# Performance work log

Measured on AMD Instinct MI355X. Metric: run time of the kernel, lower is better.

## Reference

```python
import jax, jax.numpy as jnp
import numpy as np

B, S, E = 2, 2048, 1024
H = 16
D = E // H          # head_dim = 64
W = 32              # sliding window / block size


def setup_inputs() -> dict:
    key = jax.random.key(0)
    k1, k2, k3 = jax.random.split(key, 3)
    x = jax.random.normal(k1, (B, S, E), dtype=jnp.float32)
    # xavier-uniform-like scale for the projections
    lim_qkv = float(np.sqrt(6.0 / (E + 3 * E)))
    lim_o = float(np.sqrt(6.0 / (E + E)))
    Wqkv = jax.random.uniform(k2, (3 * E, E), minval=-lim_qkv, maxval=lim_qkv, dtype=jnp.float32)
    bqkv = jnp.zeros((3 * E,), dtype=jnp.float32)
    Wo = jax.random.uniform(k3, (E, E), minval=-lim_o, maxval=lim_o, dtype=jnp.float32)
    bo = jnp.zeros((E,), dtype=jnp.float32)
    return {"x": x, "Wqkv": Wqkv, "bqkv": bqkv, "Wo": Wo, "bo": bo}


def _roll_blocks(kb, w):
    # kb: (BH, nb, w, d). Replicates roll(): w circularly-shifted copies along the
    # block axis, original inserted at index (w-1)//2, concatenated within-block.
    shifts = list(range(1, w))
    shifts.insert((w - 1) // 2, 0)
    return jnp.concatenate([jnp.roll(kb, s, axis=1) for s in shifts], axis=2)  # (BH, nb, w*w, d)


def reference(x, Wqkv, bqkv, Wo, bo):
    b, s, e = x.shape
    qkv = x @ Wqkv.T + bqkv                              # (B,S,3E)
    qkv = qkv.reshape(b, s, H, 3 * D).transpose(0, 2, 1, 3)  # (B,H,S,3D)
    q, k, v = jnp.split(qkv, 3, axis=-1)                 # each (B,H,S,D)

    nb = s // W
    qb = q.reshape(b * H, nb, W, D)
    kb = k.reshape(b * H, nb, W, D)
    kblk = _roll_blocks(kb, W)                           # (BH, nb, W*W, D)
    qk = jnp.einsum('bcxd,bcyd->bcxy', qb, kblk)         # (BH, nb, W, W*W)
    attn = qk.reshape(b, H, s, W * W) / jnp.sqrt(jnp.float32(D))
    attn = jax.nn.softmax(attn, axis=-1)
    # Faithful to torch.einsum('ijkl,ijkm->ijkm', attn, v): sum attn over its
    # last axis (==1 after softmax) and broadcast-multiply v.
    vals = attn.sum(axis=-1, keepdims=True) * v          # (B,H,S,D)

    vals = vals.transpose(0, 2, 1, 3).reshape(b, s, e)   # (B,S,E)
    return vals @ Wo.T + bo
```

## Files before the change

kernel.cpp:

```cpp
#include <hip/hip_runtime.h>
#include <hip/hip_bf16.h>
#include <type_traits>

#define MROWS 4096
#define EDIM  1024

typedef __attribute__((ext_vector_type(8))) __bf16 bf16x8;
typedef __attribute__((ext_vector_type(4))) float f32x4;
typedef __attribute__((ext_vector_type(8))) unsigned short ushort8;

__device__ __forceinline__ unsigned short f2bf(float f) {
    unsigned u = __builtin_bit_cast(unsigned, f);
    u += 0x7FFFu + ((u >> 16) & 1u);
    return (unsigned short)(u >> 16);
}

__device__ __forceinline__ void async_load16(const void* g, void* l) {
    __builtin_amdgcn_global_load_lds(
        (const __attribute__((address_space(1))) void*)g,
        (__attribute__((address_space(3))) void*)l, 16, 0, 0);
}

__device__ __forceinline__ void cast8(const float* __restrict__ in,
                                      unsigned short* __restrict__ out, int i) {
    const float4* p = (const float4*)in + (size_t)i * 2;
    float4 a = p[0], b = p[1];
    ushort8 r;
    r[0] = f2bf(a.x); r[1] = f2bf(a.y); r[2] = f2bf(a.z); r[3] = f2bf(a.w);
    r[4] = f2bf(b.x); r[5] = f2bf(b.y); r[6] = f2bf(b.z); r[7] = f2bf(b.w);
    *((ushort8*)out + i) = r;
}

template<bool BIAS, typename OUT_T, int MD, int ND, int KD,
         int BM, int BN, int BK, int NWM, int NWN>
__device__ __forceinline__ void gemm_bt_body(
    const unsigned short* __restrict__ A, const unsigned short* __restrict__ B,
    OUT_T* __restrict__ C, const float* __restrict__ bias, int id,
    unsigned short* sm)
{
    constexpr int THREADS = NWM * NWN * 64;
    constexpr int NBM = MD / BM, NBN = ND / BN, NWG = NBM * NBN;
    constexpr int CPX = NWG / 8;
    constexpr int WTM = BM / NWM, WTN = BN / NWN;
    constexpr int AM = WTM / 16, AN = WTN / 16;
    constexpr int CHUNKS = BK / 8;
    constexpr int RPP = THREADS / CHUNKS;
    constexpr int TILE = (BM + BN) * BK;

    const int t = threadIdx.x;
    const int swz = (id & 7) * CPX + (id >> 3);
    const int bm = swz % NBM, bn = swz / NBM;

    const int lane = t & 63, wave = t >> 6;
    const int wr = wave / NWN, wc = wave % NWN;

    const int rsub = t / CHUNKS;
    const int kb   = (t % CHUNKS) * 8;

    const unsigned short* Ag = A + (size_t)(bm * BM + rsub) * KD + kb;
    const unsigned short* Bg = B + (size_t)(bn * BN + rsub) * KD + kb;

    f32x4 acc[AM][AN] = {};

    auto stage = [&](int buf, int k0) {
        unsigned short* As = sm + buf * TILE;
        unsigned short* Bs = As + BM * BK;
        #pragma unroll
        for (int p = 0; p < BM / RPP; ++p)
            async_load16(Ag + (size_t)(p * RPP) * KD + k0, &As[(rsub + p * RPP) * BK + kb]);
        #pragma unroll
        for (int p = 0; p < BN / RPP; ++p)
            async_load16(Bg + (size_t)(p * RPP) * KD + k0, &Bs[(rsub + p * RPP) * BK + kb]);
    };

    auto compute = [&](int buf) {
        const unsigned short* As = sm + buf * TILE;
        const unsigned short* Bs = As + BM * BK;
        #pragma unroll
        for (int ks = 0; ks < BK / 32; ++ks) {
            bf16x8 a[AM], b[AN];
            #pragma unroll
            for (int mi = 0; mi < AM; ++mi)
                a[mi] = *(const bf16x8*)&As[(wr * WTM + mi * 16 + (lane & 15)) * BK + ks * 32 + (lane >> 4) * 8];
            #pragma unroll
            for (int ni = 0; ni < AN; ++ni)
                b[ni] = *(const bf16x8*)&Bs[(wc * WTN + ni * 16 + (lane & 15)) * BK + ks * 32 + (lane >> 4) * 8];
            #pragma unroll
            for (int mi = 0; mi < AM; ++mi)
                #pragma unroll
                for (int ni = 0; ni < AN; ++ni)
                    acc[mi][ni] = __builtin_amdgcn_mfma_f32_16x16x32_bf16(
                        a[mi], b[ni], acc[mi][ni], 0, 0, 0);
        }
    };

    stage(0, 0);
    __syncthreads();
    int cur = 0;
    for (int k0 = BK; k0 < KD; k0 += BK) {
        stage(cur ^ 1, k0);
        compute(cur);
        __syncthreads();
        cur ^= 1;
    }
    compute(cur);

    const int crow0 = bm * BM + wr * WTM + (lane >> 4) * 4;
    const int ccol0 = bn * BN + wc * WTN + (lane & 15);
    #pragma unroll
    for (int mi = 0; mi < AM; ++mi) {
        #pragma unroll
        for (int ni = 0; ni < AN; ++ni) {
            const int col = ccol0 + ni * 16;
            float bv = 0.f;
            if constexpr (BIAS) bv = bias[col];
            #pragma unroll
            for (int i = 0; i < 4; ++i) {
                const int row = crow0 + mi * 16 + i;
                float val = acc[mi][ni][i] + bv;
                if constexpr (std::is_same<OUT_T, float>::value)
                    C[(size_t)row * ND + col] = val;
                else
                    C[(size_t)row * ND + col] = f2bf(val);
            }
        }
    }
}

__global__ __launch_bounds__(256) void prep_w(
    const float* __restrict__ Wqkv, const float* __restrict__ bqkv,
    const float* __restrict__ Wo, const float* __restrict__ bo,
    unsigned short* __restrict__ WvT, unsigned short* __restrict__ wo_bf,
    float* __restrict__ c)
{
    const int blk = blockIdx.x;
    const int t = threadIdx.x;
    if (blk < 256) {
        __shared__ unsigned short tile[64][65];
        const int eBase = (blk & 15) * 64, kBase = (blk >> 4) * 64;
        const int tx = t & 63, ty = t >> 6;
        #pragma unroll
        for (int r = ty; r < 64; r += 4) {
            int k = kBase + r;
            int j = ((k >> 6) * 192) + 128 + (k & 63);
            tile[r][tx] = f2bf(Wqkv[(size_t)j * EDIM + eBase + tx]);
        }
        __syncthreads();
        #pragma unroll
        for (int r = ty; r < 64; r += 4)
            WvT[(size_t)(eBase + r) * EDIM + kBase + tx] = tile[tx][r];
    } else if (blk < 768) {
        cast8(Wo, wo_bf, (blk - 256) * 256 + t);
    } else {
        const int b = blk - 768;
        const int wave = t >> 6, lane = t & 63;
        for (int r = 0; r < 16; ++r) {
            int row = b * 64 + wave * 16 + r;
            float s = 0.f;
            #pragma unroll
            for (int kk = 0; kk < 16; ++kk) {
                int k = kk * 64 + lane;
                int j = kk * 192 + 128 + lane;
                s += Wo[(size_t)row * EDIM + k] * bqkv[j];
            }
            #pragma unroll
            for (int off = 32; off > 0; off >>= 1) s += __shfl_down(s, off);
            if (lane == 0) c[row] = s + bo[row];
        }
    }
}

__global__ __launch_bounds__(256, 2) void gemm1_castx(
    const unsigned short* __restrict__ wo_bf, const unsigned short* __restrict__ wvt,
    unsigned short* __restrict__ m_bf,
    const float* __restrict__ x, unsigned short* __restrict__ x_bf)
{
    __shared__ unsigned short smem[2 * (64 + 64) * 64];
    const int blk = blockIdx.x;
    if (blk < 256) {
        gemm_bt_body<false, unsigned short, EDIM, EDIM, EDIM, 64, 64, 64, 2, 2>(
            wo_bf, wvt, m_bf, nullptr, blk, smem);
    } else {
        cast8(x, x_bf, (blk - 256) * 256 + threadIdx.x);
    }
}

__global__ __launch_bounds__(256, 2) void gemm2(
    const unsigned short* __restrict__ x_bf, const unsigned short* __restrict__ m_bf,
    float* __restrict__ out, const float* __restrict__ cvec)
{
    __shared__ unsigned short smem[2 * (128 + 64) * 64];
    gemm_bt_body<true, float, MROWS, EDIM, EDIM, 128, 64, 64, 2, 2>(
        x_bf, m_bf, out, cvec, blockIdx.x, smem);
}

extern "C" void kernel_launch(void* const* d_in, const int* in_sizes, int n_in,
                              void* d_out, int out_size, void* d_ws, size_t ws_size,
                              hipStream_t stream) {
    const float* x    = (const float*)d_in[0];
    const float* Wqkv = (const float*)d_in[1];
    const float* bqkv = (const float*)d_in[2];
    const float* Wo   = (const float*)d_in[3];
    const float* bo   = (const float*)d_in[4];
    float* out = (float*)d_out;

    char* ws = (char*)d_ws;
    unsigned short* x_bf  = (unsigned short*)(ws);
    unsigned short* wvt   = (unsigned short*)(ws + 8u  * 1024 * 1024);
    unsigned short* wo_bf = (unsigned short*)(ws + 10u * 1024 * 1024);
    unsigned short* m_bf  = (unsigned short*)(ws + 12u * 1024 * 1024);
    float*          cvec  = (float*)(ws + 14u * 1024 * 1024);

    prep_w<<<784, 256, 0, stream>>>(Wqkv, bqkv, Wo, bo, wvt, wo_bf, cvec);
    gemm1_castx<<<2304, 256, 0, stream>>>(wo_bf, wvt, m_bf, x, x_bf);
    gemm2<<<512, 256, 0, stream>>>(x_bf, m_bf, out, cvec);
}
```

Before: 47.47 us.

## Triple-buffer GEMM LDS pipeline with explicit vmcnt waits

Replaces the double-buffered global-to-LDS load loop with a three-stage ring that issues loads two tiles ahead. It waits with explicit s_waitcnt vmcnt counts instead of __syncthreads, so later tiles stay in flight while the current one is computed. This is meant to hide global load latency behind MFMA work. In exchange LDS use per block grows by half, which may lower occupancy, and correctness depends on the hand-computed vmcnt literals matching the number of issued loads.

```diff
diff --git a/kernel.cpp b/kernel.cpp
--- a/kernel.cpp
+++ b/kernel.cpp
@@ -19,6 +19,15 @@
     __builtin_amdgcn_global_load_lds(
         (const __attribute__((address_space(1))) void*)g,
         (__attribute__((address_space(3))) void*)l, 16, 0, 0);
+}
+
+template<int N> __device__ __forceinline__ void wait_vmcnt() {
+    if constexpr (N == 0)       asm volatile("s_waitcnt vmcnt(0)" ::: "memory");
+    else if constexpr (N == 4)  asm volatile("s_waitcnt vmcnt(4)" ::: "memory");
+    else if constexpr (N == 6)  asm volatile("s_waitcnt vmcnt(6)" ::: "memory");
+    else if constexpr (N == 8)  asm volatile("s_waitcnt vmcnt(8)" ::: "memory");
+    else if constexpr (N == 12) asm volatile("s_waitcnt vmcnt(12)" ::: "memory");
+    else static_assert(N < 0, "unsupported vmcnt literal");
 }
 
 __device__ __forceinline__ void cast8(const float* __restrict__ in,
@@ -46,6 +55,8 @@
     constexpr int CHUNKS = BK / 8;
     constexpr int RPP = THREADS / CHUNKS;
     constexpr int TILE = (BM + BN) * BK;
+    constexpr int L = BM / RPP + BN / RPP;
+    constexpr int NIT = KD / BK;
 
     const int t = threadIdx.x;
     const int swz = (id & 7) * CPX + (id >> 3);
@@ -95,15 +106,21 @@
     };
 
     stage(0, 0);
-    __syncthreads();
-    int cur = 0;
-    for (int k0 = BK; k0 < KD; k0 += BK) {
-        stage(cur ^ 1, k0);
-        compute(cur);
-        __syncthreads();
-        cur ^= 1;
-    }
-    compute(cur);
+    stage(1, BK);
+
+    for (int it = 0; it < NIT; ++it) {
+        __builtin_amdgcn_s_barrier();
+        if (it + 2 < NIT) {
+            stage((it + 2) % 3, (it + 2) * BK);
+            wait_vmcnt<2 * L>();
+        } else if (it + 1 < NIT) {
+            wait_vmcnt<L>();
+        } else {
+            wait_vmcnt<0>();
+        }
+        __builtin_amdgcn_s_barrier();
+        compute(it % 3);
+    }
 
     const int crow0 = bm * BM + wr * WTM + (lane >> 4) * 4;
     const int ccol0 = bn * BN + wc * WTN + (lane & 15);
@@ -175,7 +192,7 @@
     unsigned short* __restrict__ m_bf,
     const float* __restrict__ x, unsigned short* __restrict__ x_bf)
 {
-    __shared__ unsigned short smem[2 * (64 + 64) * 64];
+    __shared__ unsigned short smem[3 * (64 + 64) * 64];
     const int blk = blockIdx.x;
     if (blk < 256) {
         gemm_bt_body<false, unsigned short, EDIM, EDIM, EDIM, 64, 64, 64, 2, 2>(
@@ -189,7 +206,7 @@
     const unsigned short* __restrict__ x_bf, const unsigned short* __restrict__ m_bf,
     float* __restrict__ out, const float* __restrict__ cvec)
 {
-    __shared__ unsigned short smem[2 * (128 + 64) * 64];
+    __shared__ unsigned short smem[3 * (128 + 64) * 64];
     gemm_bt_body<true, float, MROWS, EDIM, EDIM, 128, 64, 64, 2, 2>(
         x_bf, m_bf, out, cvec, blockIdx.x, smem);
 }
```

After: 46.41 us. 1.02x faster.
